# Performance work log

Measured on AMD Instinct MI355X. Metric: run time of the kernel, lower is better.

Reference implementation:

```python
import jax, jax.numpy as jnp
import numpy as np

EPS = 0.1
MAX_ITER = 100
THRESH = 0.1


def setup_inputs() -> dict:
    key = jax.random.key(0)
    kx, ky = jax.random.split(key)
    x = jax.random.normal(kx, (4, 2048, 64), dtype=jnp.float32)
    y = jax.random.normal(ky, (4, 2048, 64), dtype=jnp.float32)
    return {"x": x, "y": y}


def _cost_matrix(x, y, p=2):
    # |x_i - y_j|^p summed over feature dim -> (B, P1, P2)
    return jnp.sum(jnp.abs(x[..., :, None, :] - y[..., None, :, :]) ** p, axis=-1)


def _M(C, u, v, eps):
    # (-C_ij + u_i + v_j) / eps
    return (-C + u[..., :, None] + v[..., None, :]) / eps


def reference(x, y):
    C = _cost_matrix(x, y)                     # (B, P1, P2)
    B, P1 = x.shape[0], x.shape[-2]
    P2 = y.shape[-2]
    mu = jnp.full((B, P1), 1.0 / P1, dtype=jnp.float32)
    nu = jnp.full((B, P2), 1.0 / P2, dtype=jnp.float32)
    log_mu = jnp.log(mu + 1e-8)
    log_nu = jnp.log(nu + 1e-8)

    u0 = jnp.zeros_like(mu)
    v0 = jnp.zeros_like(nu)

    def step(carry, _):
        u, v, done = carry
        # torch loop: update u, then v (with new u), then check err and break
        u_new = EPS * (log_mu - jax.nn.logsumexp(_M(C, u, v, EPS), axis=-1)) + u
        v_new = EPS * (log_nu - jax.nn.logsumexp(_M(C, u_new, v, EPS), axis=-2)) + v
        err = jnp.mean(jnp.sum(jnp.abs(u_new - u), axis=-1))
        # if already converged before this iteration, freeze u,v (emulates break)
        u_out = jnp.where(done, u, u_new)
        v_out = jnp.where(done, v, v_new)
        done_out = done | (err < THRESH)
        return (u_out, v_out, done_out), None

    (u, v, _), _ = jax.lax.scan(step, (u0, v0, jnp.array(False)), None, length=MAX_ITER)

    pi = jnp.exp(_M(C, u, v, EPS))             # transport plan (B, P1, P2)
    cost = jnp.sum(pi * C, axis=(-2, -1))      # (B,)  reduction='none'
    return cost, pi, C
```

## Files before the change

kernel.cpp:

```cpp
#include <hip/hip_runtime.h>
#include <cmath>

constexpr int   B        = 4;
constexpr int   P        = 2048;
constexpr int   D        = 64;
constexpr float EPS      = 0.1f;
constexpr float THRESH   = 0.1f;
constexpr int   MAX_ITER = 100;

constexpr float LOG2E   = 1.44269504088896340736f;
constexpr float LN2     = 0.69314718055994530942f;
constexpr float SCALE   = LOG2E / EPS;
constexpr float UNSCALE = EPS * LN2;

constexpr int WS_U   = 0;
constexpr int WS_V   = 8192;
constexpr int WS_UO  = 16384;
constexpr int WS_BARX = 16384;
constexpr int WS_ERR = 24576;
constexpr int WS_FLOATS = 24712;

constexpr int NBLK = 256;
constexpr int NTHR = 512;

typedef float f32x4 __attribute__((ext_vector_type(4)));

__device__ __forceinline__ float max4(float4 a) {
    return fmaxf(fmaxf(a.x, a.y), fmaxf(a.z, a.w));
}

__device__ __forceinline__ float ld_sys_f(const float* p) {
    return __hip_atomic_load((float*)p, __ATOMIC_RELAXED, __HIP_MEMORY_SCOPE_SYSTEM);
}
__device__ __forceinline__ void st_sys_f2(float2* p, float m, float s) {
    union { float2 f; unsigned long long u; } pk;
    pk.f.x = m; pk.f.y = s;
    __hip_atomic_store((unsigned long long*)p, pk.u, __ATOMIC_RELAXED, __HIP_MEMORY_SCOPE_SYSTEM);
}
__device__ __forceinline__ float4 ld_sys_f4(const float4* p) {
    f32x4 r;
    asm volatile("global_load_dwordx4 %0, %1, off sc0 sc1\n\ts_waitcnt vmcnt(0)"
                 : "=v"(r) : "v"(p) : "memory");
    return make_float4(r.x, r.y, r.z, r.w);
}
__device__ __forceinline__ void st_sys_f4(float4* p, float4 v) {
    f32x4 t;
    t.x = v.x; t.y = v.y; t.z = v.z; t.w = v.w;
    asm volatile("global_store_dwordx4 %0, %1, off sc0 sc1"
                 :: "v"(p), "v"(t) : "memory");
}

__device__ __forceinline__ void gbar(unsigned* bar, unsigned ep) {
    asm volatile("s_waitcnt vmcnt(0)" ::: "memory");
    __syncthreads();
    if (threadIdx.x == 0) {
        const int g = blockIdx.x & 15;
        unsigned* gc   = bar + g * 32;
        unsigned* root = bar + 512;
        unsigned* rel  = bar + 544 + g * 32;
        unsigned a = __hip_atomic_fetch_add(gc, 1u, __ATOMIC_RELAXED,
                                            __HIP_MEMORY_SCOPE_SYSTEM);
        if (a == ep * 16u - 1u) {
            unsigned r = __hip_atomic_fetch_add(root, 1u, __ATOMIC_RELAXED,
                                                __HIP_MEMORY_SCOPE_SYSTEM);
            if (r == ep * 16u - 1u) {
                #pragma unroll
                for (int j = 0; j < 16; ++j)
                    __hip_atomic_store(bar + 544 + j * 32, ep, __ATOMIC_RELAXED,
                                       __HIP_MEMORY_SCOPE_SYSTEM);
            }
        }
        while (__hip_atomic_load(rel, __ATOMIC_RELAXED,
                                 __HIP_MEMORY_SCOPE_SYSTEM) < ep)
            __builtin_amdgcn_s_sleep(16);
    }
    __syncthreads();
}

__device__ __forceinline__ void lse_merge(float ma, float sa, float mb, float sb,
                                          float& M, float& S) {
    float m2 = fmaxf(ma, mb);
    S = sa * exp2f(ma - m2) + sb * exp2f(mb - m2);
    M = m2;
}

__global__ __launch_bounds__(256)
void prep_kernel(const float* __restrict__ x, const float* __restrict__ y,
                 float* __restrict__ out, float* __restrict__ ws)
{
    const int bid = blockIdx.x, tid = threadIdx.x;
    const int bb = bid >> 9, tr = (bid >> 4) & 31, tc = bid & 15;
    const int row0 = tr * 64, col0 = tc * 128;

    if (bid == 0) {
        for (int i = tid; i < WS_FLOATS; i += 256) ws[i] = 0.0f;
        if (tid < B) out[tid] = 0.0f;
    }

    __shared__ float xs[64 * 65];
    __shared__ float ys[128 * 65];
    for (int i = tid; i < 64 * 64; i += 256) {
        int r = i >> 6, d = i & 63;
        xs[r * 65 + d] = x[(size_t)(bb * P + row0 + r) * D + d];
    }
    for (int i = tid; i < 128 * 64; i += 256) {
        int c = i >> 6, d = i & 63;
        ys[c * 65 + d] = y[(size_t)(bb * P + col0 + c) * D + d];
    }
    __syncthreads();

    const int tx = tid & 15, ty = tid >> 4;
    float acc[4][8];
    #pragma unroll
    for (int j = 0; j < 4; ++j)
        #pragma unroll
        for (int i = 0; i < 8; ++i) acc[j][i] = 0.0f;

    #pragma unroll 4
    for (int k = 0; k < 64; ++k) {
        float xa[4], yb[8];
        #pragma unroll
        for (int j = 0; j < 4; ++j) xa[j] = xs[(ty * 4 + j) * 65 + k];
        #pragma unroll
        for (int i = 0; i < 8; ++i) yb[i] = ys[(tx * 8 + i) * 65 + k];
        #pragma unroll
        for (int j = 0; j < 4; ++j)
            #pragma unroll
            for (int i = 0; i < 8; ++i) {
                float d = xa[j] - yb[i];
                acc[j][i] = fmaf(d, d, acc[j][i]);
            }
    }

    float* C_out = out + B + (size_t)B * P * P;
    #pragma unroll
    for (int j = 0; j < 4; ++j) {
        size_t base = (size_t)(bb * P + row0 + ty * 4 + j) * P + col0 + tx * 8;
        float4 a0 = make_float4(acc[j][0], acc[j][1], acc[j][2], acc[j][3]);
        float4 a1 = make_float4(acc[j][4], acc[j][5], acc[j][6], acc[j][7]);
        ((float4*)&C_out[base])[0] = a0;
        ((float4*)&C_out[base])[1] = a1;
    }
}

__global__ __attribute__((amdgpu_flat_work_group_size(NTHR, NTHR),
                          amdgpu_waves_per_eu(2, 2)))
void persist_kernel(const float* C, float4* part4, float* ws, float* out)
{
    float* v2s = ws + WS_V;
    float* err = ws + WS_ERR;
    unsigned* bar = (unsigned*)(ws + WS_BARX);

    const int bid = blockIdx.x, tid = threadIdx.x;
    const int w = tid >> 6, l = tid & 63;
    const int bb = bid >> 6, rc = bid & 63;
    const int row0 = rc * 32;
    const int baserow = bb * P + row0 + w * 4;

    __shared__ float4 qm[8][128];
    __shared__ float4 qs[8][128];
    __shared__ float4 vbuf[512];
    __shared__ float  esm[8];

    const float A = EPS * __logf(1.0f / (float)P + 1e-8f);

    float4 c2[4][8];
    #pragma unroll
    for (int j = 0; j < 4; ++j) {
        const float4* Crow = (const float4*)(C + (size_t)(baserow + j) * P);
        #pragma unroll
        for (int k = 0; k < 8; ++k) {
            float4 cc = Crow[l + 64 * k];
            c2[j][k] = make_float4(-SCALE * cc.x, -SCALE * cc.y,
                                   -SCALE * cc.z, -SCALE * cc.w);
        }
    }
    #pragma unroll
    for (int j = 0; j < 4; ++j)
        #pragma unroll
        for (int k = 0; k < 8; ++k)
            asm volatile("" : "+v"(c2[j][k].x), "+v"(c2[j][k].y),
                              "+v"(c2[j][k].z), "+v"(c2[j][k].w));

    float u_old[4] = {0.0f, 0.0f, 0.0f, 0.0f};
    float u2row[4] = {0.0f, 0.0f, 0.0f, 0.0f};
    float4 v4[8];
    unsigned ep = 0;

    for (int t = 0; t < MAX_ITER; ++t) {
        {
            const float4* vg = (const float4*)(v2s + bb * P);
            vbuf[tid] = ld_sys_f4(&vg[tid]);
        }
        __syncthreads();
        #pragma unroll
        for (int k = 0; k < 8; ++k) v4[k] = vbuf[l + 64 * k];

        float dsum = 0.0f;
        #pragma unroll
        for (int j = 0; j < 4; ++j) {
            float m = -1e30f;
            #pragma unroll
            for (int k = 0; k < 8; ++k) {
                float4 tt = make_float4(v4[k].x + c2[j][k].x, v4[k].y + c2[j][k].y,
                                        v4[k].z + c2[j][k].z, v4[k].w + c2[j][k].w);
                m = fmaxf(m, max4(tt));
            }
            #pragma unroll
            for (int off = 1; off < 64; off <<= 1) m = fmaxf(m, __shfl_xor(m, off));
            float s = 0.0f;
            #pragma unroll
            for (int k = 0; k < 8; ++k) {
                s += exp2f(v4[k].x + c2[j][k].x - m) + exp2f(v4[k].y + c2[j][k].y - m)
                   + exp2f(v4[k].z + c2[j][k].z - m) + exp2f(v4[k].w + c2[j][k].w - m);
            }
            #pragma unroll
            for (int off = 1; off < 64; off <<= 1) s += __shfl_xor(s, off);
            float u_nat = A - UNSCALE * (m + log2f(s));
            u2row[j] = u_nat * SCALE;
            dsum += fabsf(u_nat - u_old[j]);
            u_old[j] = u_nat;
        }

        #pragma unroll
        for (int q = 0; q < 4; ++q) {
            #pragma unroll
            for (int h = 0; h < 2; ++h) {
                const int k = 2 * q + h;
                float4 t0 = make_float4(u2row[0] + c2[0][k].x, u2row[0] + c2[0][k].y,
                                        u2row[0] + c2[0][k].z, u2row[0] + c2[0][k].w);
                float4 t1 = make_float4(u2row[1] + c2[1][k].x, u2row[1] + c2[1][k].y,
                                        u2row[1] + c2[1][k].z, u2row[1] + c2[1][k].w);
                float4 t2 = make_float4(u2row[2] + c2[2][k].x, u2row[2] + c2[2][k].y,
                                        u2row[2] + c2[2][k].z, u2row[2] + c2[2][k].w);
                float4 t3 = make_float4(u2row[3] + c2[3][k].x, u2row[3] + c2[3][k].y,
                                        u2row[3] + c2[3][k].z, u2row[3] + c2[3][k].w);
                float4 pm, ps;
                pm.x = fmaxf(fmaxf(t0.x, t1.x), fmaxf(t2.x, t3.x));
                pm.y = fmaxf(fmaxf(t0.y, t1.y), fmaxf(t2.y, t3.y));
                pm.z = fmaxf(fmaxf(t0.z, t1.z), fmaxf(t2.z, t3.z));
                pm.w = fmaxf(fmaxf(t0.w, t1.w), fmaxf(t2.w, t3.w));
                ps.x = exp2f(t0.x - pm.x) + exp2f(t1.x - pm.x) + exp2f(t2.x - pm.x) + exp2f(t3.x - pm.x);
                ps.y = exp2f(t0.y - pm.y) + exp2f(t1.y - pm.y) + exp2f(t2.y - pm.y) + exp2f(t3.y - pm.y);
                ps.z = exp2f(t0.z - pm.z) + exp2f(t1.z - pm.z) + exp2f(t2.z - pm.z) + exp2f(t3.z - pm.z);
                ps.w = exp2f(t0.w - pm.w) + exp2f(t1.w - pm.w) + exp2f(t2.w - pm.w) + exp2f(t3.w - pm.w);
                qm[w][l + 64 * h] = pm;
                qs[w][l + 64 * h] = ps;
            }
            if (q == 0 && l == 0) esm[w] = dsum;
            __syncthreads();
            if (q == 0 && tid == 0) {
                float e = 0.0f;
                #pragma unroll
                for (int i = 0; i < 8; ++i) e += esm[i];
                atomicAdd(&err[t], e);
            }
            {
                const float* qmf = (const float*)qm;
                const float* qsf = (const float*)qs;
                float M = qmf[tid], S = qsf[tid];
                #pragma unroll
                for (int ww = 1; ww < 8; ++ww)
                    lse_merge(M, S, qmf[ww * 512 + tid], qsf[ww * 512 + tid], M, S);
                float m1 = __shfl_xor(M, 1), s1 = __shfl_xor(S, 1);
                if ((tid & 1) == 0) {
                    const int cp = 256 * q + (tid >> 1);
                    st_sys_f4(&part4[((size_t)bb * 1024 + cp) * 64 + rc],
                              make_float4(M, S, m1, s1));
                }
            }
            __syncthreads();
        }

        gbar(bar, ++ep);

        {
            const int pi_ = tid >> 5, q32 = tid & 31;
            const int gp  = bid * 16 + pi_;
            const int bb2 = gp >> 10, cp2 = gp & 1023;
            const float4* base = part4 + ((size_t)bb2 * 1024 + cp2) * 64;
            float4 a  = ld_sys_f4(base + q32);
            float4 b_ = ld_sys_f4(base + q32 + 32);
            float M0 = a.x, S0 = a.y, M1 = a.z, S1 = a.w;
            lse_merge(M0, S0, b_.x, b_.y, M0, S0);
            lse_merge(M1, S1, b_.z, b_.w, M1, S1);
            #pragma unroll
            for (int off = 16; off >= 1; off >>= 1) {
                float pm0 = __shfl_xor(M0, off), ps0 = __shfl_xor(S0, off);
                float pm1 = __shfl_xor(M1, off), ps1 = __shfl_xor(S1, off);
                lse_merge(M0, S0, pm0, ps0, M0, S0);
                lse_merge(M1, S1, pm1, ps1, M1, S1);
            }
            if (q32 == 0) {
                float v0 = (A - UNSCALE * (M0 + log2f(S0))) * SCALE;
                float v1 = (A - UNSCALE * (M1 + log2f(S1))) * SCALE;
                st_sys_f2((float2*)&v2s[bb2 * 2048 + 2 * cp2], v0, v1);
            }
        }

        gbar(bar, ++ep);

        if (ld_sys_f(&err[t]) < 4.0f * THRESH) break;
    }

    {
        {
            const float4* vg = (const float4*)(v2s + bb * P);
            vbuf[tid] = ld_sys_f4(&vg[tid]);
        }
        __syncthreads();
        #pragma unroll
        for (int k = 0; k < 8; ++k) v4[k] = vbuf[l + 64 * k];

        float* cost = out;
        float* pi   = out + B;
        float lc = 0.0f;
        #pragma unroll
        for (int j = 0; j < 4; ++j) {
            const int r = row0 + w * 4 + j;
            float4* Prow = (float4*)(pi + (size_t)(bb * P + r) * P);
            const float u2 = u2row[j];
            #pragma unroll
            for (int k = 0; k < 8; ++k) {
                float4 p, cc;
                cc.x = -UNSCALE * c2[j][k].x;
                cc.y = -UNSCALE * c2[j][k].y;
                cc.z = -UNSCALE * c2[j][k].z;
                cc.w = -UNSCALE * c2[j][k].w;
                p.x = exp2f(u2 + v4[k].x + c2[j][k].x);
                p.y = exp2f(u2 + v4[k].y + c2[j][k].y);
                p.z = exp2f(u2 + v4[k].z + c2[j][k].z);
                p.w = exp2f(u2 + v4[k].w + c2[j][k].w);
                lc = fmaf(p.x, cc.x, lc); lc = fmaf(p.y, cc.y, lc);
                lc = fmaf(p.z, cc.z, lc); lc = fmaf(p.w, cc.w, lc);
                Prow[l + 64 * k] = p;
            }
        }
        #pragma unroll
        for (int off = 1; off < 64; off <<= 1) lc += __shfl_xor(lc, off);
        __syncthreads();
        if (l == 0) esm[w] = lc;
        __syncthreads();
        if (tid == 0) {
            float e = 0.0f;
            #pragma unroll
            for (int i = 0; i < 8; ++i) e += esm[i];
            atomicAdd(&cost[bb], e);
        }
    }
}

__global__ __launch_bounds__(256, 2)
void iter_kernel(const float* __restrict__ C, float* __restrict__ part_m,
                 float* __restrict__ part_s, float* __restrict__ ws, int t)
{
    float* u2s = ws + WS_U;
    float* v2s = ws + WS_V;
    float* uo  = ws + WS_UO;
    float* err = ws + WS_ERR;
    if (t > 0 && err[t - 1] < 4.0f * THRESH) return;

    const int bid = blockIdx.x, tid = threadIdx.x;
    const int w = tid >> 6, l = tid & 63;
    const int bb = bid >> 7, rc = bid & 127;
    const int row0 = rc * 16;
    const int baserow = bb * P + row0 + w * 4;

    __shared__ float4 m_lds[4 * 512];
    __shared__ float4 s_lds[4 * 512];

    const float A = EPS * __logf(1.0f / (float)P + 1e-8f);

    const float4* vv = (const float4*)(v2s + bb * P);
    float4 v4[8];
    #pragma unroll
    for (int k = 0; k < 8; ++k) v4[k] = vv[l + 64 * k];

    float4 c2[4][8];
    #pragma unroll
    for (int j = 0; j < 4; ++j) {
        const float4* Crow = (const float4*)(C + (size_t)(baserow + j) * P);
        #pragma unroll
        for (int k = 0; k < 8; ++k) {
            float4 cc = Crow[l + 64 * k];
            c2[j][k] = make_float4(-SCALE * cc.x, -SCALE * cc.y,
                                   -SCALE * cc.z, -SCALE * cc.w);
        }
    }

    float u2row[4];
    float dsum = 0.0f;
    #pragma unroll
    for (int j = 0; j < 4; ++j) {
        float m = -1e30f;
        #pragma unroll
        for (int k = 0; k < 8; ++k) {
            float4 tt = make_float4(v4[k].x + c2[j][k].x, v4[k].y + c2[j][k].y,
                                    v4[k].z + c2[j][k].z, v4[k].w + c2[j][k].w);
            m = fmaxf(m, max4(tt));
        }
        #pragma unroll
        for (int off = 1; off < 64; off <<= 1) m = fmaxf(m, __shfl_xor(m, off));
        float s = 0.0f;
        #pragma unroll
        for (int k = 0; k < 8; ++k) {
            s += exp2f(v4[k].x + c2[j][k].x - m) + exp2f(v4[k].y + c2[j][k].y - m)
               + exp2f(v4[k].z + c2[j][k].z - m) + exp2f(v4[k].w + c2[j][k].w - m);
        }
        #pragma unroll
        for (int off = 1; off < 64; off <<= 1) s += __shfl_xor(s, off);
        float u_nat = A - UNSCALE * (m + log2f(s));
        u2row[j] = u_nat * SCALE;
        if (l == 0) {
            const int rg = baserow + j;
            dsum += fabsf(u_nat - uo[rg]);
            uo[rg]  = u_nat;
            u2s[rg] = u2row[j];
        }
    }
    if (l == 0) atomicAdd(&err[t], dsum);

    #pragma unroll
    for (int k = 0; k < 8; ++k) {
        float4 t0 = make_float4(u2row[0] + c2[0][k].x, u2row[0] + c2[0][k].y,
                                u2row[0] + c2[0][k].z, u2row[0] + c2[0][k].w);
        float4 t1 = make_float4(u2row[1] + c2[1][k].x, u2row[1] + c2[1][k].y,
                                u2row[1] + c2[1][k].z, u2row[1] + c2[1][k].w);
        float4 t2 = make_float4(u2row[2] + c2[2][k].x, u2row[2] + c2[2][k].y,
                                u2row[2] + c2[2][k].z, u2row[2] + c2[2][k].w);
        float4 t3 = make_float4(u2row[3] + c2[3][k].x, u2row[3] + c2[3][k].y,
                                u2row[3] + c2[3][k].z, u2row[3] + c2[3][k].w);
        float4 pm, ps;
        pm.x = fmaxf(fmaxf(t0.x, t1.x), fmaxf(t2.x, t3.x));
        pm.y = fmaxf(fmaxf(t0.y, t1.y), fmaxf(t2.y, t3.y));
        pm.z = fmaxf(fmaxf(t0.z, t1.z), fmaxf(t2.z, t3.z));
        pm.w = fmaxf(fmaxf(t0.w, t1.w), fmaxf(t2.w, t3.w));
        ps.x = exp2f(t0.x - pm.x) + exp2f(t1.x - pm.x) + exp2f(t2.x - pm.x) + exp2f(t3.x - pm.x);
        ps.y = exp2f(t0.y - pm.y) + exp2f(t1.y - pm.y) + exp2f(t2.y - pm.y) + exp2f(t3.y - pm.y);
        ps.z = exp2f(t0.z - pm.z) + exp2f(t1.z - pm.z) + exp2f(t2.z - pm.z) + exp2f(t3.z - pm.z);
        ps.w = exp2f(t0.w - pm.w) + exp2f(t1.w - pm.w) + exp2f(t2.w - pm.w) + exp2f(t3.w - pm.w);
        m_lds[w * 512 + l + 64 * k] = pm;
        s_lds[w * 512 + l + 64 * k] = ps;
    }
    __syncthreads();

    float4* pm_out = ((float4*)part_m) + (size_t)bid * 512;
    float4* ps_out = ((float4*)part_s) + (size_t)bid * 512;
    #pragma unroll
    for (int h = 0; h < 2; ++h) {
        const int idx = tid * 2 + h;
        float4 M = m_lds[idx], S = s_lds[idx];
        #pragma unroll
        for (int q = 1; q < 4; ++q) {
            float4 pm = m_lds[q * 512 + idx], ps = s_lds[q * 512 + idx];
            float m2;
            m2 = fmaxf(M.x, pm.x); S.x = S.x * exp2f(M.x - m2) + ps.x * exp2f(pm.x - m2); M.x = m2;
            m2 = fmaxf(M.y, pm.y); S.y = S.y * exp2f(M.y - m2) + ps.y * exp2f(pm.y - m2); M.y = m2;
            m2 = fmaxf(M.z, pm.z); S.z = S.z * exp2f(M.z - m2) + ps.z * exp2f(pm.z - m2); M.z = m2;
            m2 = fmaxf(M.w, pm.w); S.w = S.w * exp2f(M.w - m2) + ps.w * exp2f(pm.w - m2); M.w = m2;
        }
        pm_out[idx] = M;
        ps_out[idx] = S;
    }
}

__global__ __launch_bounds__(256)
void comb_kernel(const float* __restrict__ part_m, const float* __restrict__ part_s,
                 float* __restrict__ ws, int t)
{
    float* v2s = ws + WS_V;
    float* err = ws + WS_ERR;
    if (t > 0 && err[t - 1] < 4.0f * THRESH) return;

    const int g = blockIdx.x * 256 + threadIdx.x;
    const int b = g >> 11, c = g & (P - 1);
    const float* pmb = part_m + (size_t)(b * 128) * P + c;
    const float* psb = part_s + (size_t)(b * 128) * P + c;

    const float A = EPS * __logf(1.0f / (float)P + 1e-8f);

    float M = -1e30f;
    #pragma unroll 8
    for (int q = 0; q < 128; ++q) M = fmaxf(M, pmb[(size_t)q * P]);
    float S = 0.0f;
    #pragma unroll 8
    for (int q = 0; q < 128; ++q)
        S = fmaf(psb[(size_t)q * P], exp2f(pmb[(size_t)q * P] - M), S);

    float v_nat = A - UNSCALE * (M + log2f(S));
    v2s[g] = v_nat * SCALE;
}

__global__ __launch_bounds__(256)
void epi_kernel(float* __restrict__ out, const float* __restrict__ ws)
{
    const float* u2s = ws + WS_U;
    const float* v2s = ws + WS_V;
    float* cost = out;
    float* pi   = out + B;
    const float* C = out + B + (size_t)B * P * P;

    const int bid = blockIdx.x, tid = threadIdx.x;
    const int w = tid >> 6, l = tid & 63;
    const int bb = bid >> 7, rc = bid & 127;
    const int row0 = rc * 16;

    const float4* vv = (const float4*)(v2s + bb * P);
    float4 v4[8];
    #pragma unroll
    for (int k = 0; k < 8; ++k) v4[k] = vv[l + 64 * k];

    float lc = 0.0f;
    #pragma unroll
    for (int j = 0; j < 4; ++j) {
        const int r = row0 + w * 4 + j;
        const float u2 = u2s[bb * P + r];
        const float4* Crow = (const float4*)(C  + (size_t)(bb * P + r) * P);
        float4*       Prow = (float4*)      (pi + (size_t)(bb * P + r) * P);
        #pragma unroll
        for (int k = 0; k < 8; ++k) {
            float4 cc = Crow[l + 64 * k];
            float4 p;
            p.x = exp2f(u2 + v4[k].x - SCALE * cc.x);
            p.y = exp2f(u2 + v4[k].y - SCALE * cc.y);
            p.z = exp2f(u2 + v4[k].z - SCALE * cc.z);
            p.w = exp2f(u2 + v4[k].w - SCALE * cc.w);
            lc = fmaf(p.x, cc.x, lc); lc = fmaf(p.y, cc.y, lc);
            lc = fmaf(p.z, cc.z, lc); lc = fmaf(p.w, cc.w, lc);
            Prow[l + 64 * k] = p;
        }
    }
    #pragma unroll
    for (int off = 1; off < 64; off <<= 1) lc += __shfl_xor(lc, off);
    __shared__ float sm[4];
    if (l == 0) sm[w] = lc;
    __syncthreads();
    if (tid == 0) atomicAdd(&cost[bb], sm[0] + sm[1] + sm[2] + sm[3]);
}

extern "C" void kernel_launch(void* const* d_in, const int* in_sizes, int n_in,
                              void* d_out, int out_size, void* d_ws, size_t ws_size,
                              hipStream_t stream) {
    const float* x = (const float*)d_in[0];
    const float* y = (const float*)d_in[1];
    float* out = (float*)d_out;
    float* ws  = (float*)d_ws;
    const float* C = out + B + (size_t)B * P * P;
    float4* part4 = (float4*)(out + B);
    float* part_m = out + B;
    float* part_s = part_m + 512 * P;

    prep_kernel<<<2048, 256, 0, stream>>>(x, y, out, ws);

    void* args[] = { (void*)&C, (void*)&part4, (void*)&ws, (void*)&out };
    hipError_t e = hipLaunchCooperativeKernel((void*)persist_kernel,
                                              dim3(NBLK), dim3(NTHR),
                                              args, 0, stream);
    if (e != hipSuccess) {
        for (int t = 0; t < MAX_ITER; ++t) {
            iter_kernel<<<512, 256, 0, stream>>>(C, part_m, part_s, ws, t);
            comb_kernel<<<32,  256, 0, stream>>>(part_m, part_s, ws, t);
        }
        epi_kernel<<<512, 256, 0, stream>>>(out, ws);
    }
}
```

Measured before the change: 2.150 ms.

## Double persistent block threads to 1024 with two rows per wave

Raises the persistent kernel to 1024 threads per block, so each wave holds two cost-matrix rows in registers instead of four. The column-partial merge and the cross-block reduction are reworked to match: one wave per column pair, 64-lane shuffle reduction, and a 4-lane split of the shared-memory LSE combine. The error flag is now read once by thread 0 inside the barrier and broadcast through shared memory, and the barrier spin sleep is shortened. The aim is more waves per CU to hide exp and latency, and less barrier overhead, at the cost of extra shuffle and shared-memory merge work.

```diff
diff --git a/kernel.cpp b/kernel.cpp
--- a/kernel.cpp
+++ b/kernel.cpp
@@ -21,7 +21,7 @@
 constexpr int WS_FLOATS = 24712;
 
 constexpr int NBLK = 256;
-constexpr int NTHR = 512;
+constexpr int NTHR = 1024;
 
 typedef float f32x4 __attribute__((ext_vector_type(4)));
 
@@ -50,29 +50,40 @@
                  :: "v"(p), "v"(t) : "memory");
 }
 
+__device__ __forceinline__ void gbar_core(unsigned* bar, unsigned ep) {
+    const int g = blockIdx.x & 15;
+    unsigned* gc   = bar + g * 32;
+    unsigned* root = bar + 512;
+    unsigned* rel  = bar + 544 + g * 32;
+    unsigned a = __hip_atomic_fetch_add(gc, 1u, __ATOMIC_RELAXED,
+                                        __HIP_MEMORY_SCOPE_SYSTEM);
+    if (a == ep * 16u - 1u) {
+        unsigned r = __hip_atomic_fetch_add(root, 1u, __ATOMIC_RELAXED,
+                                            __HIP_MEMORY_SCOPE_SYSTEM);
+        if (r == ep * 16u - 1u) {
+            #pragma unroll
+            for (int j = 0; j < 16; ++j)
+                __hip_atomic_store(bar + 544 + j * 32, ep, __ATOMIC_RELAXED,
+                                   __HIP_MEMORY_SCOPE_SYSTEM);
+        }
+    }
+    while (__hip_atomic_load(rel, __ATOMIC_RELAXED,
+                             __HIP_MEMORY_SCOPE_SYSTEM) < ep)
+        __builtin_amdgcn_s_sleep(4);
+}
 __device__ __forceinline__ void gbar(unsigned* bar, unsigned ep) {
     asm volatile("s_waitcnt vmcnt(0)" ::: "memory");
     __syncthreads();
+    if (threadIdx.x == 0) gbar_core(bar, ep);
+    __syncthreads();
+}
+__device__ __forceinline__ void gbar_err(unsigned* bar, unsigned ep,
+                                         const float* errp, float* flag) {
+    asm volatile("s_waitcnt vmcnt(0)" ::: "memory");
+    __syncthreads();
     if (threadIdx.x == 0) {
-        const int g = blockIdx.x & 15;
-        unsigned* gc   = bar + g * 32;
-        unsigned* root = bar + 512;
-        unsigned* rel  = bar + 544 + g * 32;
-        unsigned a = __hip_atomic_fetch_add(gc, 1u, __ATOMIC_RELAXED,
-                                            __HIP_MEMORY_SCOPE_SYSTEM);
-        if (a == ep * 16u - 1u) {
-            unsigned r = __hip_atomic_fetch_add(root, 1u, __ATOMIC_RELAXED,
-                                                __HIP_MEMORY_SCOPE_SYSTEM);
-            if (r == ep * 16u - 1u) {
-                #pragma unroll
-                for (int j = 0; j < 16; ++j)
-                    __hip_atomic_store(bar + 544 + j * 32, ep, __ATOMIC_RELAXED,
-                                       __HIP_MEMORY_SCOPE_SYSTEM);
-            }
-        }
-        while (__hip_atomic_load(rel, __ATOMIC_RELAXED,
-                                 __HIP_MEMORY_SCOPE_SYSTEM) < ep)
-            __builtin_amdgcn_s_sleep(16);
+        gbar_core(bar, ep);
+        *flag = ld_sys_f(errp);
     }
     __syncthreads();
 }
@@ -144,7 +155,7 @@
 }
 
 __global__ __attribute__((amdgpu_flat_work_group_size(NTHR, NTHR),
-                          amdgpu_waves_per_eu(2, 2)))
+                          amdgpu_waves_per_eu(4, 4)))
 void persist_kernel(const float* C, float4* part4, float* ws, float* out)
 {
     float* v2s = ws + WS_V;
@@ -155,18 +166,19 @@
     const int w = tid >> 6, l = tid & 63;
     const int bb = bid >> 6, rc = bid & 63;
     const int row0 = rc * 32;
-    const int baserow = bb * P + row0 + w * 4;
-
-    __shared__ float4 qm[8][128];
-    __shared__ float4 qs[8][128];
+    const int baserow = bb * P + row0 + w * 2;
+
+    __shared__ float4 qm[16][128];
+    __shared__ float4 qs[16][128];
     __shared__ float4 vbuf[512];
-    __shared__ float  esm[8];
+    __shared__ float  esm[16];
+    __shared__ float  dflag;
 
     const float A = EPS * __logf(1.0f / (float)P + 1e-8f);
 
-    float4 c2[4][8];
-    #pragma unroll
-    for (int j = 0; j < 4; ++j) {
+    float4 c2[2][8];
+    #pragma unroll
+    for (int j = 0; j < 2; ++j) {
         const float4* Crow = (const float4*)(C + (size_t)(baserow + j) * P);
         #pragma unroll
         for (int k = 0; k < 8; ++k) {
@@ -176,19 +188,19 @@
         }
     }
     #pragma unroll
-    for (int j = 0; j < 4; ++j)
+    for (int j = 0; j < 2; ++j)
         #pragma unroll
         for (int k = 0; k < 8; ++k)
             asm volatile("" : "+v"(c2[j][k].x), "+v"(c2[j][k].y),
                               "+v"(c2[j][k].z), "+v"(c2[j][k].w));
 
-    float u_old[4] = {0.0f, 0.0f, 0.0f, 0.0f};
-    float u2row[4] = {0.0f, 0.0f, 0.0f, 0.0f};
+    float u_old[2] = {0.0f, 0.0f};
+    float u2row[2] = {0.0f, 0.0f};
     float4 v4[8];
     unsigned ep = 0;
 
     for (int t = 0; t < MAX_ITER; ++t) {
-        {
+        if (tid < 512) {
             const float4* vg = (const float4*)(v2s + bb * P);
             vbuf[tid] = ld_sys_f4(&vg[tid]);
         }
@@ -198,7 +210,7 @@
 
         float dsum = 0.0f;
         #pragma unroll
-        for (int j = 0; j < 4; ++j) {
+        for (int j = 0; j < 2; ++j) {
             float m = -1e30f;
             #pragma unroll
             for (int k = 0; k < 8; ++k) {
@@ -221,6 +233,7 @@
             dsum += fabsf(u_nat - u_old[j]);
             u_old[j] = u_nat;
         }
+        if (l == 0) esm[w] = dsum;
 
         #pragma unroll
         for (int q = 0; q < 4; ++q) {
@@ -231,40 +244,39 @@
                                         u2row[0] + c2[0][k].z, u2row[0] + c2[0][k].w);
                 float4 t1 = make_float4(u2row[1] + c2[1][k].x, u2row[1] + c2[1][k].y,
                                         u2row[1] + c2[1][k].z, u2row[1] + c2[1][k].w);
-                float4 t2 = make_float4(u2row[2] + c2[2][k].x, u2row[2] + c2[2][k].y,
-                                        u2row[2] + c2[2][k].z, u2row[2] + c2[2][k].w);
-                float4 t3 = make_float4(u2row[3] + c2[3][k].x, u2row[3] + c2[3][k].y,
-                                        u2row[3] + c2[3][k].z, u2row[3] + c2[3][k].w);
                 float4 pm, ps;
-                pm.x = fmaxf(fmaxf(t0.x, t1.x), fmaxf(t2.x, t3.x));
-                pm.y = fmaxf(fmaxf(t0.y, t1.y), fmaxf(t2.y, t3.y));
-                pm.z = fmaxf(fmaxf(t0.z, t1.z), fmaxf(t2.z, t3.z));
-                pm.w = fmaxf(fmaxf(t0.w, t1.w), fmaxf(t2.w, t3.w));
-                ps.x = exp2f(t0.x - pm.x) + exp2f(t1.x - pm.x) + exp2f(t2.x - pm.x) + exp2f(t3.x - pm.x);
-                ps.y = exp2f(t0.y - pm.y) + exp2f(t1.y - pm.y) + exp2f(t2.y - pm.y) + exp2f(t3.y - pm.y);
-                ps.z = exp2f(t0.z - pm.z) + exp2f(t1.z - pm.z) + exp2f(t2.z - pm.z) + exp2f(t3.z - pm.z);
-                ps.w = exp2f(t0.w - pm.w) + exp2f(t1.w - pm.w) + exp2f(t2.w - pm.w) + exp2f(t3.w - pm.w);
+                pm.x = fmaxf(t0.x, t1.x); pm.y = fmaxf(t0.y, t1.y);
+                pm.z = fmaxf(t0.z, t1.z); pm.w = fmaxf(t0.w, t1.w);
+                ps.x = exp2f(t0.x - pm.x) + exp2f(t1.x - pm.x);
+                ps.y = exp2f(t0.y - pm.y) + exp2f(t1.y - pm.y);
+                ps.z = exp2f(t0.z - pm.z) + exp2f(t1.z - pm.z);
+                ps.w = exp2f(t0.w - pm.w) + exp2f(t1.w - pm.w);
                 qm[w][l + 64 * h] = pm;
                 qs[w][l + 64 * h] = ps;
             }
-            if (q == 0 && l == 0) esm[w] = dsum;
             __syncthreads();
             if (q == 0 && tid == 0) {
                 float e = 0.0f;
                 #pragma unroll
-                for (int i = 0; i < 8; ++i) e += esm[i];
+                for (int i = 0; i < 16; ++i) e += esm[i];
                 atomicAdd(&err[t], e);
             }
             {
                 const float* qmf = (const float*)qm;
                 const float* qsf = (const float*)qs;
-                float M = qmf[tid], S = qsf[tid];
+                const int col = tid >> 1, p = tid & 1;
+                float M = qmf[(p * 8) * 512 + col], S = qsf[(p * 8) * 512 + col];
                 #pragma unroll
                 for (int ww = 1; ww < 8; ++ww)
-                    lse_merge(M, S, qmf[ww * 512 + tid], qsf[ww * 512 + tid], M, S);
-                float m1 = __shfl_xor(M, 1), s1 = __shfl_xor(S, 1);
-                if ((tid & 1) == 0) {
-                    const int cp = 256 * q + (tid >> 1);
+                    lse_merge(M, S, qmf[(p * 8 + ww) * 512 + col],
+                              qsf[(p * 8 + ww) * 512 + col], M, S);
+                {
+                    float pm = __shfl_xor(M, 1), psv = __shfl_xor(S, 1);
+                    lse_merge(M, S, pm, psv, M, S);
+                }
+                float m1 = __shfl_xor(M, 2), s1 = __shfl_xor(S, 2);
+                if ((tid & 3) == 0) {
+                    const int cp = 256 * q + (tid >> 2);
                     st_sys_f4(&part4[((size_t)bb * 1024 + cp) * 64 + rc],
                               make_float4(M, S, m1, s1));
                 }
@@ -275,36 +287,30 @@
         gbar(bar, ++ep);
 
         {
-            const int pi_ = tid >> 5, q32 = tid & 31;
-            const int gp  = bid * 16 + pi_;
+            const int gp  = bid * 16 + w;
             const int bb2 = gp >> 10, cp2 = gp & 1023;
-            const float4* base = part4 + ((size_t)bb2 * 1024 + cp2) * 64;
-            float4 a  = ld_sys_f4(base + q32);
-            float4 b_ = ld_sys_f4(base + q32 + 32);
+            float4 a = ld_sys_f4(part4 + ((size_t)bb2 * 1024 + cp2) * 64 + l);
             float M0 = a.x, S0 = a.y, M1 = a.z, S1 = a.w;
-            lse_merge(M0, S0, b_.x, b_.y, M0, S0);
-            lse_merge(M1, S1, b_.z, b_.w, M1, S1);
-            #pragma unroll
-            for (int off = 16; off >= 1; off >>= 1) {
+            #pragma unroll
+            for (int off = 32; off >= 1; off >>= 1) {
                 float pm0 = __shfl_xor(M0, off), ps0 = __shfl_xor(S0, off);
                 float pm1 = __shfl_xor(M1, off), ps1 = __shfl_xor(S1, off);
                 lse_merge(M0, S0, pm0, ps0, M0, S0);
                 lse_merge(M1, S1, pm1, ps1, M1, S1);
             }
-            if (q32 == 0) {
+            if (l == 0) {
                 float v0 = (A - UNSCALE * (M0 + log2f(S0))) * SCALE;
                 float v1 = (A - UNSCALE * (M1 + log2f(S1))) * SCALE;
                 st_sys_f2((float2*)&v2s[bb2 * 2048 + 2 * cp2], v0, v1);
             }
         }
 
-        gbar(bar, ++ep);
-
-        if (ld_sys_f(&err[t]) < 4.0f * THRESH) break;
+        gbar_err(bar, ++ep, &err[t], &dflag);
+        if (dflag < 4.0f * THRESH) break;
     }
 
     {
-        {
+        if (tid < 512) {
             const float4* vg = (const float4*)(v2s + bb * P);
             vbuf[tid] = ld_sys_f4(&vg[tid]);
         }
@@ -316,8 +322,8 @@
         float* pi   = out + B;
         float lc = 0.0f;
         #pragma unroll
-        for (int j = 0; j < 4; ++j) {
-            const int r = row0 + w * 4 + j;
+        for (int j = 0; j < 2; ++j) {
+            const int r = row0 + w * 2 + j;
             float4* Prow = (float4*)(pi + (size_t)(bb * P + r) * P);
             const float u2 = u2row[j];
             #pragma unroll
@@ -344,7 +350,7 @@
         if (tid == 0) {
             float e = 0.0f;
             #pragma unroll
-            for (int i = 0; i < 8; ++i) e += esm[i];
+            for (int i = 0; i < 16; ++i) e += esm[i];
             atomicAdd(&cost[bb], e);
         }
     }
```

Result: slower. 3.094 ms (+43.9%).
